# Kernel optimization log

Hardware: AMD Instinct MI355X
Metric: run time of the kernel (lower is better)

## Reference

```python
import jax, jax.numpy as jnp
import numpy as np

T, B, D = 1024, 128, 512
CLIP = 1.0  # grad_clip_value


def setup_inputs() -> dict:
    key = jax.random.key(0)
    ks = jax.random.split(key, 6)
    s = 1.0 / np.sqrt(D)
    return {
        "h0": jnp.zeros((B, D), jnp.float32),
        "ins": jax.random.normal(ks[0], (T, B, D), jnp.float32),
        "resets": jax.random.bernoulli(ks[1], 0.05, (T, B)),
        # GRUCell params: input kernels (with bias) for r,z,n fused; hidden kernels
        # for r,z (no bias, per flax GRUCell) fused; hidden kernel for n (with bias).
        "Wi": (jax.random.normal(ks[2], (D, 3 * D), jnp.float32) * s),
        "bi": jnp.zeros((3 * D,), jnp.float32),
        "Wh_rz": (jax.random.normal(ks[3], (D, 2 * D), jnp.float32) * s),
        "Whn": (jax.random.normal(ks[4], (D, D), jnp.float32) * s),
        "bhn": jnp.zeros((D,), jnp.float32),
    }


def reference(h0, ins, resets, Wi, bi, Wh_rz, Whn, bhn):
    def st_clip(x):
        # straight-through clip: forward = clip(x), backward = identity
        return x + jax.lax.stop_gradient(jnp.clip(x, -CLIP, CLIP) - x)

    def step(h, xt):
        x, reset = xt                      # x: [B,D], reset: [B]
        h = jnp.where(reset[:, None], 0.0, h)  # reset carry to zeros
        gi = x @ Wi + bi                   # [B,3D]
        grz = h @ Wh_rz                    # [B,2D]
        r = jax.nn.sigmoid(gi[:, :D] + grz[:, :D])
        z = jax.nn.sigmoid(gi[:, D:2 * D] + grz[:, D:])
        n = jnp.tanh(gi[:, 2 * D:] + r * (h @ Whn + bhn))
        h_new = (1.0 - z) * n + z * h      # GRU update; y == new carry in flax
        h_new = st_clip(h_new)
        return h_new, h_new

    _, ys = jax.lax.scan(step, h0, (ins, resets))
    return ys  # [T,B,D]
```

## Files before the change

### kernel.cpp

```cpp
#include <hip/hip_runtime.h>
#include <stdint.h>


typedef float f32x4 __attribute__((ext_vector_type(4)));
typedef short s16x8 __attribute__((ext_vector_type(8)));

#define DD 512
#define BB 128
#define TT 1024

static __device__ __forceinline__ unsigned short f2bf(float f) {
  uint32_t u = __builtin_bit_cast(uint32_t, f);
  u = (u + 0x7fffu + ((u >> 16) & 1u)) >> 16;
  return (unsigned short)u;
}
static __device__ __forceinline__ float b2f(uint32_t bits) {
  return __builtin_bit_cast(float, bits << 16);
}
static __device__ __forceinline__ s16x8 ldsfrag(const char* p) {
  return __builtin_bit_cast(s16x8, *reinterpret_cast<const uint4*>(p));
}

__global__ void prep(const float* __restrict__ Wi, const float* __restrict__ Whrz,
                     const float* __restrict__ Whn,
                     unsigned short* __restrict__ Wipk, unsigned short* __restrict__ Wpk) {
  int i = blockIdx.x * 256 + threadIdx.x;
  if (i < 786432) {
    int ck = i >> 9, k = i & 511;
    int cj = ck / 96, c96 = ck % 96;
    int g = c96 >> 5, cc = c96 & 31;
    Wipk[i] = f2bf(Wi[(size_t)k * 1536 + g * 512 + cj * 32 + cc]);
  } else {
    int j = i - 786432;
    int ck = j >> 9, k = j & 511;
    int cj = ck / 96, c96 = ck % 96;
    int g = c96 >> 5, cc = c96 & 31;
    float v = (g < 2) ? Whrz[(size_t)k * 1024 + g * 512 + cj * 32 + cc]
                      : Whn[(size_t)k * 512 + cj * 32 + cc];
    Wpk[j] = f2bf(v);
  }
}

__global__ void tag0(const float* __restrict__ h0, uint32_t* __restrict__ hxt,
                     float* __restrict__ hbF) {
  int i = blockIdx.x * 512 + threadIdx.x;
  float v = h0[i];
  hxt[i] = (uint32_t)f2bf(v);
  hbF[i] = v;
}

__global__ void scanR(const int* __restrict__ r, int* __restrict__ flag) {
  int i = blockIdx.x * 256 + threadIdx.x;
  unsigned int v = (unsigned int)r[i];
  if (v > 1u) atomicOr(flag, 1);
}

static __device__ __forceinline__ unsigned rmask16f(const int* resets, int rmode,
                                                    long long tg, int row0) {
  unsigned m = 0;
  if (rmode) {
    const unsigned char* rb = reinterpret_cast<const unsigned char*>(resets);
    uint4 u = *reinterpret_cast<const uint4*>(rb + (size_t)tg * 128 + row0);
    unsigned w0 = u.x, w1 = u.y, w2 = u.z, w3 = u.w;
#pragma unroll
    for (int b = 0; b < 4; ++b) {
      if ((w0 >> (8 * b)) & 0xFFu) m |= 1u << (0 + b);
      if ((w1 >> (8 * b)) & 0xFFu) m |= 1u << (4 + b);
      if ((w2 >> (8 * b)) & 0xFFu) m |= 1u << (8 + b);
      if ((w3 >> (8 * b)) & 0xFFu) m |= 1u << (12 + b);
    }
  } else {
    const uint4* p = reinterpret_cast<const uint4*>(resets + (size_t)tg * 128 + row0);
#pragma unroll
    for (int q = 0; q < 4; ++q) {
      uint4 u = p[q];
      if (u.x) m |= 1u << (q * 4 + 0);
      if (u.y) m |= 1u << (q * 4 + 1);
      if (u.z) m |= 1u << (q * 4 + 2);
      if (u.w) m |= 1u << (q * 4 + 3);
    }
  }
  return m;
}

static __device__ __forceinline__ void pollTag(const uint32_t* src, unsigned exp,
                                               unsigned short (&v)[16]) {
  bool need = true;
  for (int it = 0; it < (1 << 12); ++it) {
    if (need) {
      uint32_t u[16];
#pragma unroll
      for (int i = 0; i < 16; ++i)
        u[i] = __hip_atomic_load(src + (size_t)i * 512,
                                 __ATOMIC_RELAXED, __HIP_MEMORY_SCOPE_AGENT);
      unsigned bad = 0;
#pragma unroll
      for (int i = 0; i < 16; ++i) bad |= ((u[i] >> 16) ^ exp);
      if (bad == 0u) {
#pragma unroll
        for (int i = 0; i < 16; ++i) v[i] = (unsigned short)u[i];
        need = false;
      }
    }
    if (__ballot(need ? 1 : 0) == 0ull) break;
    if (it >= 1) __builtin_amdgcn_s_sleep(1);
  }
}

#define RNN_SMEM (16384 + 16384 + 34816)

__global__ __launch_bounds__(512) void rnnB(const float* __restrict__ x,
                                            const unsigned short* __restrict__ Wipk,
                                            const unsigned short* __restrict__ Wpk,
                                            const float* __restrict__ bi,
                                            const float* __restrict__ bhn,
                                            const int* __restrict__ resets,
                                            uint32_t* hxt,
                                            const float* __restrict__ hbF,
                                            const int* __restrict__ rmodep,
                                            float* __restrict__ ys,
                                            int tc) {
  extern __shared__ char smem[];
  char* Hlb = smem;
  char* Xlb = smem + 16384;
  float* ax = reinterpret_cast<float*>(smem + 32768);

  const int tid = threadIdx.x;
  const int lane = tid & 63;
  const int wv = tid >> 6;
  const int w = wv & 1, ks = wv >> 1;
  const int cj = blockIdx.x >> 3, rg = blockIdx.x & 7;
  const int ec = tid & 31, eb = tid >> 5;
  const int bglob = rg * 16 + eb;
  const int colglob = cj * 32 + ec;
  const int rmode = *rmodep;

  uint4 wreg[3][4], wireg[3][4];
  {
    const size_t fb = (size_t)cj * 96 * 512
                    + (size_t)(w * 16 + (lane & 15)) * 512
                    + ks * 128 + (lane >> 4) * 8;
#pragma unroll
    for (int g = 0; g < 3; ++g)
#pragma unroll
      for (int kk = 0; kk < 4; ++kk) {
        wreg[g][kk]  = *reinterpret_cast<const uint4*>(Wpk  + fb + g * 32 * 512 + kk * 32);
        wireg[g][kk] = *reinterpret_cast<const uint4*>(Wipk + fb + g * 32 * 512 + kk * 32);
      }
  }

  const float bhn_c = bhn[colglob];
  float bir3[3];
#pragma unroll
  for (int g = 0; g < 3; ++g) bir3[g] = bi[g * 512 + colglob];
  float h_old = hbF[(size_t)bglob * 512 + colglob];

  unsigned short v[16];
  pollTag(hxt + (size_t)rg * 8192 + tid, 0u, v);
  unsigned mask = rmask16f(resets, rmode, 0, rg * 16);

  float xa[16];
#pragma unroll
  for (int i = 0; i < 16; ++i)
    xa[i] = x[(size_t)(rg * 16 + i) * 512 + tid];

  int soff[16];
#pragma unroll
  for (int i = 0; i < 16; ++i)
    soff[i] = i * 1024 + (((((tid * 2) >> 4) ^ (i & 7)) << 4) | ((tid & 7) * 2));

  for (int t = 0; t < tc; ++t) {
    float xaN[16];
    const bool haveN = (t + 1 < tc);
    if (haveN) {
#pragma unroll
      for (int i = 0; i < 16; ++i)
        xaN[i] = x[((size_t)(t + 1) * 128 + rg * 16 + i) * 512 + tid];
    }
#pragma unroll
    for (int i = 0; i < 16; ++i) {
      unsigned short hv = ((mask >> i) & 1u) ? (unsigned short)0 : v[i];
      *reinterpret_cast<unsigned short*>(Hlb + soff[i]) = hv;
      *reinterpret_cast<unsigned short*>(Xlb + soff[i]) = f2bf(xa[i]);
    }
    __syncthreads();
    f32x4 accR = (f32x4){0.f, 0.f, 0.f, 0.f};
    f32x4 accZ = accR, accNX = accR, accNH = accR;
    {
      const int rowb = lane & 15;
      const int hsw = (rowb & 7) << 4;
      const int kplusB = (lane >> 4) << 4;
      s16x8 hfrag[4], xfrag[4];
#pragma unroll
      for (int kk = 0; kk < 4; ++kk) {
        const int kbB = (ks * 128 + kk * 32) * 2 + kplusB;
        hfrag[kk] = ldsfrag(Hlb + rowb * 1024 + (kbB ^ hsw));
        xfrag[kk] = ldsfrag(Xlb + rowb * 1024 + (kbB ^ hsw));
      }
#pragma unroll
      for (int kk = 0; kk < 4; ++kk) {
        accR = __builtin_amdgcn_mfma_f32_16x16x32_bf16(
            __builtin_bit_cast(s16x8, wireg[0][kk]), xfrag[kk], accR, 0, 0, 0);
        accZ = __builtin_amdgcn_mfma_f32_16x16x32_bf16(
            __builtin_bit_cast(s16x8, wireg[1][kk]), xfrag[kk], accZ, 0, 0, 0);
        accNX = __builtin_amdgcn_mfma_f32_16x16x32_bf16(
            __builtin_bit_cast(s16x8, wireg[2][kk]), xfrag[kk], accNX, 0, 0, 0);
        accR = __builtin_amdgcn_mfma_f32_16x16x32_bf16(
            __builtin_bit_cast(s16x8, wreg[0][kk]), hfrag[kk], accR, 0, 0, 0);
        accZ = __builtin_amdgcn_mfma_f32_16x16x32_bf16(
            __builtin_bit_cast(s16x8, wreg[1][kk]), hfrag[kk], accZ, 0, 0, 0);
        accNH = __builtin_amdgcn_mfma_f32_16x16x32_bf16(
            __builtin_bit_cast(s16x8, wreg[2][kk]), hfrag[kk], accNH, 0, 0, 0);
      }
    }
    {
      const int mh = (lane >> 4) << 2, nn = lane & 15;
      float* base = ax + (size_t)((ks * 2 + w) * 4) * 272 + nn;
#pragma unroll
      for (int r = 0; r < 4; ++r) {
        base[(mh + r) * 17] = accR[r];
        base[272 + (mh + r) * 17] = accZ[r];
        base[544 + (mh + r) * 17] = accNX[r];
        base[816 + (mh + r) * 17] = accNH[r];
      }
    }
    __syncthreads();
    {
      const int wc = ec >> 4, mc = ec & 15;
      float s0 = 0.f, s1 = 0.f, s2x = 0.f, s2h = 0.f;
#pragma unroll
      for (int k2 = 0; k2 < 4; ++k2) {
        const float* p = ax + (size_t)((k2 * 2 + wc) * 4) * 272 + mc * 17 + eb;
        s0 += p[0]; s1 += p[272]; s2x += p[544]; s2h += p[816];
      }
      const float r = 1.f / (1.f + __expf(-(bir3[0] + s0)));
      const float z = 1.f / (1.f + __expf(-(bir3[1] + s1)));
      const float hu = ((mask >> eb) & 1u) ? 0.f : h_old;
      const float pre = (bir3[2] + s2x) + r * (s2h + bhn_c);
      const float n = 1.f - 2.f / (1.f + __expf(2.f * pre));
      float hn = (1.f - z) * n + z * hu;
      hn = fminf(1.f, fmaxf(-1.f, hn));
      const uint32_t tagged = (((uint32_t)(t + 1) & 0xFFFFu) << 16) | (uint32_t)f2bf(hn);
      __hip_atomic_store(hxt + (size_t)((t + 1) & 1) * 65536 + (size_t)bglob * 512 + colglob,
                         tagged, __ATOMIC_RELAXED, __HIP_MEMORY_SCOPE_AGENT);
      __builtin_nontemporal_store(hn, ys + ((size_t)t * 128 + bglob) * 512 + colglob);
      h_old = hn;
    }
    if (haveN) {
      unsigned nmask = rmask16f(resets, rmode, t + 1, rg * 16);
      pollTag(hxt + (size_t)((t + 1) & 1) * 65536 + (size_t)rg * 8192 + tid,
              (unsigned)(t + 1) & 0xFFFFu, v);
      mask = nmask;
#pragma unroll
      for (int i = 0; i < 16; ++i) xa[i] = xaN[i];
    }
  }
}

extern "C" void kernel_launch(void* const* d_in, const int* in_sizes, int n_in,
                              void* d_out, int out_size, void* d_ws, size_t ws_size,
                              hipStream_t stream) {
  const float* h0 = (const float*)d_in[0];
  const float* ins = (const float*)d_in[1];
  const int* rst = (const int*)d_in[2];
  const float* Wi = (const float*)d_in[3];
  const float* bi = (const float*)d_in[4];
  const float* Whrz = (const float*)d_in[5];
  const float* Whn = (const float*)d_in[6];
  const float* bhn = (const float*)d_in[7];
  float* ys = (float*)d_out;

  char* ws = (char*)d_ws;
  unsigned short* Wpk = (unsigned short*)(ws);
  unsigned short* Wipk = (unsigned short*)(ws + 1572864);
  uint32_t* hxt = (uint32_t*)(ws + 3145728);
  float* hbF = (float*)(ws + 3670016);
  int* flag = (int*)(ws + 3932160);

  hipMemsetAsync(flag, 0, 4, stream);
  hipMemsetAsync(hxt, 0, 524288, stream);
  tag0<<<dim3(128), dim3(512), 0, stream>>>(h0, hxt, hbF);
  prep<<<dim3(6144), dim3(256), 0, stream>>>(Wi, Whrz, Whn, Wipk, Wpk);
  scanR<<<dim3(128), dim3(256), 0, stream>>>(rst, flag);
  hipFuncSetAttribute((const void*)rnnB, hipFuncAttributeMaxDynamicSharedMemorySize,
                      RNN_SMEM);
  rnnB<<<dim3(128), dim3(512), RNN_SMEM, stream>>>(ins, Wipk, Wpk, bi, bhn, rst,
                                                   hxt, hbF, flag, ys, 1024);
}
```

Measured before the change: 3.516 ms.

## Precompute next-step input projection before polling and vectorize h exchange loads

Moves the x@Wi MFMA work for step t+1 off the serial critical path by computing it after the current step's h store and before polling for the next h. The polling now reads contiguous 64-bit words (16 consecutive columns per thread) instead of 16 strided 32-bit atomics, and x/h are written to LDS as packed 16-byte stores. It adds an extra __syncthreads per step and changes the thread-to-data mapping for LDS staging. The poll iteration limit is also raised.

```diff
diff --git a/kernel.cpp b/kernel.cpp
--- a/kernel.cpp
+++ b/kernel.cpp
@@ -13,9 +13,6 @@
   uint32_t u = __builtin_bit_cast(uint32_t, f);
   u = (u + 0x7fffu + ((u >> 16) & 1u)) >> 16;
   return (unsigned short)u;
-}
-static __device__ __forceinline__ float b2f(uint32_t bits) {
-  return __builtin_bit_cast(float, bits << 16);
 }
 static __device__ __forceinline__ s16x8 ldsfrag(const char* p) {
   return __builtin_bit_cast(s16x8, *reinterpret_cast<const uint4*>(p));
@@ -83,28 +80,37 @@
   return m;
 }
 
-static __device__ __forceinline__ void pollTag(const uint32_t* src, unsigned exp,
-                                               unsigned short (&v)[16]) {
+static __device__ __forceinline__ void pollTagQ(const uint32_t* src, unsigned exp,
+                                                unsigned short (&v)[16]) {
+  const unsigned long long* s8 = reinterpret_cast<const unsigned long long*>(src);
   bool need = true;
-  for (int it = 0; it < (1 << 12); ++it) {
+  for (int it = 0; it < (1 << 14); ++it) {
     if (need) {
-      uint32_t u[16];
-#pragma unroll
-      for (int i = 0; i < 16; ++i)
-        u[i] = __hip_atomic_load(src + (size_t)i * 512,
-                                 __ATOMIC_RELAXED, __HIP_MEMORY_SCOPE_AGENT);
+      unsigned long long q[8];
+#pragma unroll
+      for (int i = 0; i < 8; ++i)
+        q[i] = __hip_atomic_load(s8 + i, __ATOMIC_RELAXED, __HIP_MEMORY_SCOPE_AGENT);
       unsigned bad = 0;
 #pragma unroll
-      for (int i = 0; i < 16; ++i) bad |= ((u[i] >> 16) ^ exp);
+      for (int i = 0; i < 8; ++i)
+        bad |= (unsigned)(((q[i] >> 16) ^ (unsigned long long)exp) & 0xFFFFull)
+             | (unsigned)(((q[i] >> 48) ^ (unsigned long long)exp) & 0xFFFFull);
       if (bad == 0u) {
 #pragma unroll
-        for (int i = 0; i < 16; ++i) v[i] = (unsigned short)u[i];
+        for (int i = 0; i < 8; ++i) {
+          v[2 * i]     = (unsigned short)q[i];
+          v[2 * i + 1] = (unsigned short)(q[i] >> 32);
+        }
         need = false;
       }
     }
     if (__ballot(need ? 1 : 0) == 0ull) break;
     if (it >= 1) __builtin_amdgcn_s_sleep(1);
   }
+}
+
+static __device__ __forceinline__ f32x4 mfbf(uint4 wfr, s16x8 b, f32x4 c) {
+  return __builtin_amdgcn_mfma_f32_16x16x32_bf16(__builtin_bit_cast(s16x8, wfr), b, c, 0, 0, 0);
 }
 
 #define RNN_SMEM (16384 + 16384 + 34816)
@@ -133,7 +139,15 @@
   const int ec = tid & 31, eb = tid >> 5;
   const int bglob = rg * 16 + eb;
   const int colglob = cj * 32 + ec;
+  const int b16 = tid & 15, seg = tid >> 4;
+  const int swzB = (b16 & 7) << 4;
+  const int soff0 = b16 * 1024 + ((seg * 32) ^ swzB);
+  const int soff1 = b16 * 1024 + ((seg * 32 + 16) ^ swzB);
   const int rmode = *rmodep;
+
+  const int rowb = lane & 15;
+  const int hsw = (rowb & 7) << 4;
+  const int kplusB = (lane >> 4) << 4;
 
   uint4 wreg[3][4], wireg[3][4];
   {
@@ -155,73 +169,91 @@
   for (int g = 0; g < 3; ++g) bir3[g] = bi[g * 512 + colglob];
   float h_old = hbF[(size_t)bglob * 512 + colglob];
 
+  float4 xq[4];
+  {
+    const float* xr = x + (size_t)(rg * 16 + b16) * 512 + seg * 16;
+#pragma unroll
+    for (int q = 0; q < 4; ++q) xq[q] = *reinterpret_cast<const float4*>(xr + q * 4);
+  }
+  {
+    uint4 p0, p1;
+    p0.x = (uint32_t)f2bf(xq[0].x) | ((uint32_t)f2bf(xq[0].y) << 16);
+    p0.y = (uint32_t)f2bf(xq[0].z) | ((uint32_t)f2bf(xq[0].w) << 16);
+    p0.z = (uint32_t)f2bf(xq[1].x) | ((uint32_t)f2bf(xq[1].y) << 16);
+    p0.w = (uint32_t)f2bf(xq[1].z) | ((uint32_t)f2bf(xq[1].w) << 16);
+    p1.x = (uint32_t)f2bf(xq[2].x) | ((uint32_t)f2bf(xq[2].y) << 16);
+    p1.y = (uint32_t)f2bf(xq[2].z) | ((uint32_t)f2bf(xq[2].w) << 16);
+    p1.z = (uint32_t)f2bf(xq[3].x) | ((uint32_t)f2bf(xq[3].y) << 16);
+    p1.w = (uint32_t)f2bf(xq[3].z) | ((uint32_t)f2bf(xq[3].w) << 16);
+    *reinterpret_cast<uint4*>(Xlb + soff0) = p0;
+    *reinterpret_cast<uint4*>(Xlb + soff1) = p1;
+  }
+  __syncthreads();
+  f32x4 xpR = (f32x4){0.f, 0.f, 0.f, 0.f}, xpZ = xpR, xpN = xpR;
+  {
+    s16x8 xf[4];
+#pragma unroll
+    for (int kk = 0; kk < 4; ++kk) {
+      const int kbB = (ks * 128 + kk * 32) * 2 + kplusB;
+      xf[kk] = ldsfrag(Xlb + rowb * 1024 + (kbB ^ hsw));
+    }
+#pragma unroll
+    for (int kk = 0; kk < 4; ++kk) {
+      xpR = mfbf(wireg[0][kk], xf[kk], xpR);
+      xpZ = mfbf(wireg[1][kk], xf[kk], xpZ);
+      xpN = mfbf(wireg[2][kk], xf[kk], xpN);
+    }
+  }
+  if (tc > 1) {
+    const float* xr = x + ((size_t)1 * 128 + rg * 16 + b16) * 512 + seg * 16;
+#pragma unroll
+    for (int q = 0; q < 4; ++q) xq[q] = *reinterpret_cast<const float4*>(xr + q * 4);
+  }
   unsigned short v[16];
-  pollTag(hxt + (size_t)rg * 8192 + tid, 0u, v);
+  pollTagQ(hxt + (size_t)(rg * 16 + b16) * 512 + seg * 16, 0u, v);
   unsigned mask = rmask16f(resets, rmode, 0, rg * 16);
 
-  float xa[16];
-#pragma unroll
-  for (int i = 0; i < 16; ++i)
-    xa[i] = x[(size_t)(rg * 16 + i) * 512 + tid];
-
-  int soff[16];
-#pragma unroll
-  for (int i = 0; i < 16; ++i)
-    soff[i] = i * 1024 + (((((tid * 2) >> 4) ^ (i & 7)) << 4) | ((tid & 7) * 2));
-
   for (int t = 0; t < tc; ++t) {
-    float xaN[16];
-    const bool haveN = (t + 1 < tc);
-    if (haveN) {
-#pragma unroll
-      for (int i = 0; i < 16; ++i)
-        xaN[i] = x[((size_t)(t + 1) * 128 + rg * 16 + i) * 512 + tid];
-    }
-#pragma unroll
-    for (int i = 0; i < 16; ++i) {
-      unsigned short hv = ((mask >> i) & 1u) ? (unsigned short)0 : v[i];
-      *reinterpret_cast<unsigned short*>(Hlb + soff[i]) = hv;
-      *reinterpret_cast<unsigned short*>(Xlb + soff[i]) = f2bf(xa[i]);
+    {
+      const unsigned keep = ((mask >> b16) & 1u) ? 0u : 0xFFFFFFFFu;
+      uint4 p0, p1;
+      p0.x = ((uint32_t)v[0] | ((uint32_t)v[1] << 16)) & keep;
+      p0.y = ((uint32_t)v[2] | ((uint32_t)v[3] << 16)) & keep;
+      p0.z = ((uint32_t)v[4] | ((uint32_t)v[5] << 16)) & keep;
+      p0.w = ((uint32_t)v[6] | ((uint32_t)v[7] << 16)) & keep;
+      p1.x = ((uint32_t)v[8] | ((uint32_t)v[9] << 16)) & keep;
+      p1.y = ((uint32_t)v[10] | ((uint32_t)v[11] << 16)) & keep;
+      p1.z = ((uint32_t)v[12] | ((uint32_t)v[13] << 16)) & keep;
+      p1.w = ((uint32_t)v[14] | ((uint32_t)v[15] << 16)) & keep;
+      *reinterpret_cast<uint4*>(Hlb + soff0) = p0;
+      *reinterpret_cast<uint4*>(Hlb + soff1) = p1;
     }
     __syncthreads();
-    f32x4 accR = (f32x4){0.f, 0.f, 0.f, 0.f};
-    f32x4 accZ = accR, accNX = accR, accNH = accR;
+    f32x4 hR = (f32x4){0.f, 0.f, 0.f, 0.f}, hZ = hR, hNH = hR;
     {
-      const int rowb = lane & 15;
-      const int hsw = (rowb & 7) << 4;
-      const int kplusB = (lane >> 4) << 4;
-      s16x8 hfrag[4], xfrag[4];
+      s16x8 hf[4];
 #pragma unroll
       for (int kk = 0; kk < 4; ++kk) {
         const int kbB = (ks * 128 + kk * 32) * 2 + kplusB;
-        hfrag[kk] = ldsfrag(Hlb + rowb * 1024 + (kbB ^ hsw));
-        xfrag[kk] = ldsfrag(Xlb + rowb * 1024 + (kbB ^ hsw));
+        hf[kk] = ldsfrag(Hlb + rowb * 1024 + (kbB ^ hsw));
       }
 #pragma unroll
       for (int kk = 0; kk < 4; ++kk) {
-        accR = __builtin_amdgcn_mfma_f32_16x16x32_bf16(
-            __builtin_bit_cast(s16x8, wireg[0][kk]), xfrag[kk], accR, 0, 0, 0);
-        accZ = __builtin_amdgcn_mfma_f32_16x16x32_bf16(
-            __builtin_bit_cast(s16x8, wireg[1][kk]), xfrag[kk], accZ, 0, 0, 0);
-        accNX = __builtin_amdgcn_mfma_f32_16x16x32_bf16(
-            __builtin_bit_cast(s16x8, wireg[2][kk]), xfrag[kk], accNX, 0, 0, 0);
-        accR = __builtin_amdgcn_mfma_f32_16x16x32_bf16(
-            __builtin_bit_cast(s16x8, wreg[0][kk]), hfrag[kk], accR, 0, 0, 0);
-        accZ = __builtin_amdgcn_mfma_f32_16x16x32_bf16(
-            __builtin_bit_cast(s16x8, wreg[1][kk]), hfrag[kk], accZ, 0, 0, 0);
-        accNH = __builtin_amdgcn_mfma_f32_16x16x32_bf16(
-            __builtin_bit_cast(s16x8, wreg[2][kk]), hfrag[kk], accNH, 0, 0, 0);
+        hR = mfbf(wreg[0][kk], hf[kk], hR);
+        hZ = mfbf(wreg[1][kk], hf[kk], hZ);
+        hNH = mfbf(wreg[2][kk], hf[kk], hNH);
       }
     }
     {
       const int mh = (lane >> 4) << 2, nn = lane & 15;
       float* base = ax + (size_t)((ks * 2 + w) * 4) * 272 + nn;
+      const f32x4 pR = hR + xpR, pZ = hZ + xpZ;
 #pragma unroll
       for (int r = 0; r < 4; ++r) {
-        base[(mh + r) * 17] = accR[r];
-        base[272 + (mh + r) * 17] = accZ[r];
-        base[544 + (mh + r) * 17] = accNX[r];
-        base[816 + (mh + r) * 17] = accNH[r];
+        base[(mh + r) * 17] = pR[r];
+        base[272 + (mh + r) * 17] = pZ[r];
+        base[544 + (mh + r) * 17] = xpN[r];
+        base[816 + (mh + r) * 17] = hNH[r];
       }
     }
     __syncthreads();
@@ -246,13 +278,45 @@
       __builtin_nontemporal_store(hn, ys + ((size_t)t * 128 + bglob) * 512 + colglob);
       h_old = hn;
     }
-    if (haveN) {
-      unsigned nmask = rmask16f(resets, rmode, t + 1, rg * 16);
-      pollTag(hxt + (size_t)((t + 1) & 1) * 65536 + (size_t)rg * 8192 + tid,
-              (unsigned)(t + 1) & 0xFFFFu, v);
+    if (t + 1 < tc) {
+      const unsigned nmask = rmask16f(resets, rmode, t + 1, rg * 16);
+      {
+        uint4 p0, p1;
+        p0.x = (uint32_t)f2bf(xq[0].x) | ((uint32_t)f2bf(xq[0].y) << 16);
+        p0.y = (uint32_t)f2bf(xq[0].z) | ((uint32_t)f2bf(xq[0].w) << 16);
+        p0.z = (uint32_t)f2bf(xq[1].x) | ((uint32_t)f2bf(xq[1].y) << 16);
+        p0.w = (uint32_t)f2bf(xq[1].z) | ((uint32_t)f2bf(xq[1].w) << 16);
+        p1.x = (uint32_t)f2bf(xq[2].x) | ((uint32_t)f2bf(xq[2].y) << 16);
+        p1.y = (uint32_t)f2bf(xq[2].z) | ((uint32_t)f2bf(xq[2].w) << 16);
+        p1.z = (uint32_t)f2bf(xq[3].x) | ((uint32_t)f2bf(xq[3].y) << 16);
+        p1.w = (uint32_t)f2bf(xq[3].z) | ((uint32_t)f2bf(xq[3].w) << 16);
+        *reinterpret_cast<uint4*>(Xlb + soff0) = p0;
+        *reinterpret_cast<uint4*>(Xlb + soff1) = p1;
+      }
+      __syncthreads();
+      {
+        s16x8 xf[4];
+#pragma unroll
+        for (int kk = 0; kk < 4; ++kk) {
+          const int kbB = (ks * 128 + kk * 32) * 2 + kplusB;
+          xf[kk] = ldsfrag(Xlb + rowb * 1024 + (kbB ^ hsw));
+        }
+        xpR = (f32x4){0.f, 0.f, 0.f, 0.f}; xpZ = xpR; xpN = xpR;
+#pragma unroll
+        for (int kk = 0; kk < 4; ++kk) {
+          xpR = mfbf(wireg[0][kk], xf[kk], xpR);
+          xpZ = mfbf(wireg[1][kk], xf[kk], xpZ);
+          xpN = mfbf(wireg[2][kk], xf[kk], xpN);
+        }
+      }
+      if (t + 2 < tc) {
+        const float* xr = x + ((size_t)(t + 2) * 128 + rg * 16 + b16) * 512 + seg * 16;
+#pragma unroll
+        for (int q = 0; q < 4; ++q) xq[q] = *reinterpret_cast<const float4*>(xr + q * 4);
+      }
+      pollTagQ(hxt + (size_t)((t + 1) & 1) * 65536 + (size_t)(rg * 16 + b16) * 512 + seg * 16,
+               (unsigned)(t + 1) & 0xFFFFu, v);
       mask = nmask;
-#pragma unroll
-      for (int i = 0; i < 16; ++i) xa[i] = xaN[i];
     }
   }
 }
```

Measured after the change: 4.902 ms. +39.4%, slower.
